# Performance work log

Measured on AMD Instinct MI355X. Metric: run time of the kernel, lower is better.

## Reference

```python
import jax, jax.numpy as jnp
import numpy as np

N_NODES = 16384
N_EDGES = 262144
N_GRAPHS = 64
H = 256          # hidden_dim
DE = 192         # edge feature dim
DG = 64          # g_all dim (DE + DG == H)
NITERS = 3


def _lin(key, fan_in, fan_out):
    kw, kb = jax.random.split(key)
    s = 1.0 / np.sqrt(fan_in)
    return (jax.random.uniform(kw, (fan_in, fan_out), jnp.float32, -s, s),
            jax.random.uniform(kb, (fan_out,), jnp.float32, -s, s))


def setup_inputs() -> dict:
    key = jax.random.key(0)
    ks = jax.random.split(key, 12)
    edge_features = jax.random.normal(ks[0], (N_EDGES, DE), jnp.float32)
    g_all = jax.random.normal(ks[1], (1, DG), jnp.float32)
    edge_index = jax.random.randint(ks[2], (2, N_EDGES), 0, N_NODES, jnp.int32)
    # node_degrees: in-degree per node (what the 1/(1+deg) normalization expects)
    node_degrees = jax.ops.segment_sum(jnp.ones((N_EDGES,), jnp.int32), edge_index[1], num_segments=N_NODES)
    # 64 graphs of 256 nodes each (sorted segment ids, no empty graphs)
    batch = jnp.repeat(jnp.arange(N_GRAPHS, dtype=jnp.int32), N_NODES // N_GRAPHS)
    offs = jnp.arange(N_GRAPHS, dtype=jnp.int32) * (N_NODES // N_GRAPHS)
    heads = offs + jax.random.randint(ks[3], (N_GRAPHS,), 0, N_NODES // N_GRAPHS, jnp.int32)
    tails = offs + jax.random.randint(ks[4], (N_GRAPHS,), 0, N_NODES // N_GRAPHS, jnp.int32)
    ea_w1, ea_b1 = _lin(ks[5], H, H)
    ea_w2, ea_b2 = _lin(ks[6], H, 1)
    eu_w1, eu_b1 = _lin(ks[7], 3 * H + 4, H)
    eu_w2, eu_b2 = _lin(ks[8], H, H)
    gw_w1, gw_b1 = _lin(ks[9], 3 * H, H)
    gw_w2, gw_b2 = _lin(ks[10], H, 1)
    ew_w, ew_b = _lin(ks[11], H, 1)
    return dict(edge_features=edge_features, g_all=g_all,
                ea_w1=ea_w1, ea_b1=ea_b1, ea_w2=ea_w2, ea_b2=ea_b2,
                eu_w1=eu_w1, eu_b1=eu_b1, eu_w2=eu_w2, eu_b2=eu_b2,
                gw_w1=gw_w1, gw_b1=gw_b1, gw_w2=gw_w2, gw_b2=gw_b2,
                ew_w=ew_w, ew_b=ew_b,
                edge_index=edge_index, node_degrees=node_degrees,
                batch=batch, heads=heads, tails=tails)


def reference(edge_features, g_all, ea_w1, ea_b1, ea_w2, ea_b2,
              eu_w1, eu_b1, eu_w2, eu_b2, gw_w1, gw_b1, gw_w2, gw_b2,
              ew_w, ew_b, edge_index, node_degrees, batch, heads, tails):
    src, recv = edge_index[0], edge_index[1]
    E = src.shape[0]
    N = node_degrees.shape[0]
    n_graphs = heads.shape[0]
    dt = edge_features.dtype

    # b_e = cat([edge_features, g_all expanded over edges])
    b_e = jnp.concatenate([edge_features, jnp.broadcast_to(g_all, (E, g_all.shape[1]))], axis=1)

    node_ids = jnp.arange(N)
    is_head = (node_ids == heads[batch]).astype(dt)[:, None]
    is_tail = (node_ids == tails[batch]).astype(dt)[:, None]
    deg = node_degrees.astype(dt)[:, None]

    b_v = jnp.zeros((N, b_e.shape[1]), dt)
    for _ in range(NITERS):
        # per-edge attention score
        score = jax.nn.sigmoid(jax.nn.relu(b_e @ ea_w1 + ea_b1) @ ea_w2 + ea_b2)  # [E,1]
        # scatter_softmax over receiver segments
        m = jax.ops.segment_max(score, recv, num_segments=N)
        ex = jnp.exp(score - m[recv])
        s = jax.ops.segment_sum(ex, recv, num_segments=N)
        alpha = ex / s[recv]
        # scatter_add aggregation + degree normalization
        b_v = jax.ops.segment_sum(alpha * b_e, recv, num_segments=N) / (1.0 + deg)  # [N,H]
        # role-augmented node states, gathered back to edges
        r_v = jnp.concatenate([b_v, is_head, is_tail], axis=1)  # [N,H+2]
        msg = jnp.concatenate([r_v[src], r_v[recv], b_e], axis=1)  # [E,3H+4]
        b_e = jax.nn.relu(msg @ eu_w1 + eu_b1) @ eu_w2 + eu_b2  # [E,H]

    g_max = jax.ops.segment_max(b_v, batch, num_segments=n_graphs)  # [G,H]
    g_G = jnp.concatenate([g_max, b_v[heads], b_v[tails]], axis=1)  # [G,3H]
    w_k = jax.nn.softmax(jax.nn.relu(g_G @ gw_w1 + gw_b1) @ gw_w2 + gw_b2, axis=0)  # [G,1]
    g_all_out = jnp.sum(w_k * g_G, axis=0, keepdims=True)  # [1,3H]
    w_e = jax.nn.sigmoid(b_e @ ew_w + ew_b)  # [E,1]
    return (w_e, g_all_out)
```

## Files before the change

### kernel.cpp

```cpp
#include <hip/hip_runtime.h>
#include <stdint.h>

typedef unsigned short u16;
typedef unsigned int   u32;

#define NN 16384
#define NE 262144
#define NG 64
#define HD 256
#define SHS 264

typedef __attribute__((ext_vector_type(8))) short bfrag;
typedef __attribute__((ext_vector_type(4))) float ffrag;

__device__ __forceinline__ float bf2f(u16 h){
  union { u32 u; float f; } v; v.u = ((u32)h) << 16; return v.f;
}
__device__ __forceinline__ u16 f2bf(float x){
  union { float f; u32 u; } v; v.f = x;
  u32 r = v.u + 0x7fffu + ((v.u >> 16) & 1u);
  return (u16)(r >> 16);
}
__device__ __forceinline__ float sigmoidf(float x){ return 1.f/(1.f+__expf(-x)); }

__device__ __forceinline__ void dma16(const void* g, void* l){
  __builtin_amdgcn_global_load_lds(
      (const __attribute__((address_space(1))) u32*)g,
      (__attribute__((address_space(3))) u32*)l, 16, 0, 0);
}


enum { MODE_SCORE=0, MODE_PQ=4 };

template<int MODE>
__global__ __launch_bounds__(256, 4)
void gemm_k(const u16* __restrict__ A, const u16* __restrict__ Bf0,
            const u16* __restrict__ Bf1,
            float* __restrict__ outF, u16* __restrict__ out0, u16* __restrict__ out1,
            const float* __restrict__ bias, const float* __restrict__ vec,
            const float* __restrict__ scal, const float* __restrict__ flags,
            const float* __restrict__ ht0, const float* __restrict__ ht1)
{
  __shared__ __align__(16) u16 sA[16384];
  __shared__ float sred[4][64];

  const int l  = threadIdx.x & 63;
  const int w  = threadIdx.x >> 6;
  const int q  = l >> 4;
  const int ml = l & 15;
  const long rowBase = (long)blockIdx.x * 64;

  const u16* Bf   = Bf0;
  u16*       outB = out0;
  const float* htp = ht0;
  const float* bp  = bias;
  if (MODE==MODE_PQ && blockIdx.y){ Bf = Bf1; outB = out1; htp = ht1; bp = nullptr; }

  const u16* gA = A + (size_t)(rowBase + w*16 + ml)*HD + q*8;
#pragma unroll
  for (int c=0; c<8; ++c) dma16(gA + c*32, sA + (c*4+w)*512);

  ffrag acc[4][4];
  if constexpr (MODE==MODE_SCORE){
#pragma unroll
    for (int n=0; n<4; ++n){
      const float bb = bias[(w*4+n)*16+ml];
#pragma unroll
      for (int mt=0; mt<4; ++mt) acc[mt][n] = (ffrag){bb,bb,bb,bb};
    }
  } else {
    float h0[4], h1[4], bb[4];
#pragma unroll
    for (int n=0; n<4; ++n){
      const int col = (w*4+n)*16+ml;
      h0[n] = htp[col]; h1[n] = htp[HD+col]; bb[n] = bp ? bp[col] : 0.f;
    }
    float2 fl[16];
#pragma unroll
    for (int i=0; i<16; ++i){
      long row = rowBase + (i>>2)*16 + q*4 + (i&3);
      fl[i] = *(const float2*)(flags + 2*row);
    }
#pragma unroll
    for (int i=0; i<16; ++i){
      const int mt = i>>2, r = i&3;
      const float fh = fl[i].x, ft = fl[i].y;
#pragma unroll
      for (int n=0; n<4; ++n)
        acc[mt][n][r] = bb[n] + fh*h0[n] + ft*h1[n];
    }
  }
  __syncthreads();

  __builtin_amdgcn_s_setprio(1);
#pragma unroll 1
  for (int c=0; c<8; ++c){
    bfrag a[4], b[4];
#pragma unroll
    for (int n=0; n<4; ++n)
      b[n] = *(const bfrag*)(Bf + (((size_t)c*16 + w*4 + n)*64 + l)*8);
#pragma unroll
    for (int mt=0; mt<4; ++mt) a[mt] = *(const bfrag*)(sA + (c*4+mt)*512 + l*8);
#pragma unroll
    for (int mt=0; mt<4; ++mt)
#pragma unroll
      for (int n=0; n<4; ++n)
        acc[mt][n] = __builtin_amdgcn_mfma_f32_16x16x32_bf16(a[mt], b[n], acc[mt][n], 0, 0, 0);
  }
  __builtin_amdgcn_s_setprio(0);

  if constexpr (MODE==MODE_SCORE){
    float part[4][4];
#pragma unroll
    for (int mt=0; mt<4; ++mt)
#pragma unroll
      for (int r=0; r<4; ++r) part[mt][r] = 0.f;
#pragma unroll
    for (int n=0; n<4; ++n){
      const float vvn = vec[(w*4+n)*16+ml];
#pragma unroll
      for (int mt=0; mt<4; ++mt)
#pragma unroll
        for (int r=0; r<4; ++r)
          part[mt][r] += fmaxf(acc[mt][n][r], 0.f) * vvn;
    }
#pragma unroll
    for (int mt=0; mt<4; ++mt)
#pragma unroll
      for (int r=0; r<4; ++r){
        float p = part[mt][r];
        p += __shfl_xor(p, 1, 64); p += __shfl_xor(p, 2, 64);
        p += __shfl_xor(p, 4, 64); p += __shfl_xor(p, 8, 64);
        part[mt][r] = p;
      }
    if (ml == 0)
#pragma unroll
      for (int mt=0; mt<4; ++mt)
#pragma unroll
        for (int r=0; r<4; ++r)
          sred[w][mt*16 + q*4 + r] = part[mt][r];
    __syncthreads();
    if (threadIdx.x < 64){
      const int t = threadIdx.x;
      float v = sred[0][t] + sred[1][t] + sred[2][t] + sred[3][t];
      outF[rowBase + t] = sigmoidf(v + scal[0]);
    }
  } else {
#pragma unroll
    for (int mt=0; mt<4; ++mt)
#pragma unroll
      for (int r=0; r<4; ++r){
        long row = rowBase + mt*16 + q*4 + r;
        u16 o[4];
#pragma unroll
        for (int n=0; n<4; ++n) o[n] = f2bf(acc[mt][n][r]);
        uint2 pk; pk.x = (u32)o[0] | ((u32)o[1]<<16); pk.y = (u32)o[2] | ((u32)o[3]<<16);
        *(uint2*)(outB + (size_t)row*HD + w*64 + ml*4) = pk;
      }
  }
}

template<bool LAST>
__global__ __launch_bounds__(256, 4)
void mega_k(u16* __restrict__ BE, const u16* __restrict__ w1cf,
            const u16* __restrict__ w2f, const u16* __restrict__ eaw1f,
            float* __restrict__ scoreOut, float* __restrict__ weOut,
            const u16* __restrict__ Pg, const u16* __restrict__ Qg,
            const int* __restrict__ srcI, const int* __restrict__ recvI,
            const float* __restrict__ b2,
            const float* __restrict__ sb1, const float* __restrict__ sv,
            const float* __restrict__ ssc,
            const float* __restrict__ wv, const float* __restrict__ wb)
{
  __shared__ __align__(16) u16 sU[64*SHS];
  __shared__ float sred[4][64];
  __shared__ int sIdx[128];

  const int l  = threadIdx.x & 63;
  const int w  = threadIdx.x >> 6;
  const int q  = l >> 4;
  const int ml = l & 15;
  const long rowBase = (long)blockIdx.x * 64;

  const u16* gA = BE + (size_t)(rowBase + w*16 + ml)*HD + q*8;
#pragma unroll
  for (int c=0; c<8; ++c) dma16(gA + c*32, sU + (c*4+w)*512);
  __syncthreads();

  if (threadIdx.x < 128){
    const int t = threadIdx.x;
    sIdx[t] = (t < 64) ? srcI[rowBase + t] : recvI[rowBase + (t - 64)];
  }

  ffrag acc[4][4];
#pragma unroll
  for (int mt=0; mt<4; ++mt)
#pragma unroll
    for (int n=0; n<4; ++n) acc[mt][n] = (ffrag){0.f,0.f,0.f,0.f};

  __builtin_amdgcn_s_setprio(1);
#pragma unroll 1
  for (int c=0; c<8; ++c){
    bfrag a[4], b[4];
#pragma unroll
    for (int n=0; n<4; ++n)
      b[n] = *(const bfrag*)(w1cf + (((size_t)c*16 + w*4 + n)*64 + l)*8);
#pragma unroll
    for (int mt=0; mt<4; ++mt) a[mt] = *(const bfrag*)(sU + (c*4+mt)*512 + l*8);
#pragma unroll
    for (int mt=0; mt<4; ++mt)
#pragma unroll
      for (int n=0; n<4; ++n)
        acc[mt][n] = __builtin_amdgcn_mfma_f32_16x16x32_bf16(a[mt], b[n], acc[mt][n], 0, 0, 0);
  }
  __builtin_amdgcn_s_setprio(0);
  __syncthreads();

#pragma unroll
  for (int mt=0; mt<4; ++mt)
#pragma unroll
    for (int r=0; r<4; ++r){
      const int rl = mt*16 + q*4 + r;
      const int si = sIdx[rl];
      const int ri = sIdx[64 + rl];
      uint2 pu = *(const uint2*)(Pg + (size_t)si*HD + w*64 + ml*4);
      uint2 qu = *(const uint2*)(Qg + (size_t)ri*HD + w*64 + ml*4);
      u16 o[4];
      float pv[4] = { bf2f((u16)(pu.x & 0xffff)), bf2f((u16)(pu.x >> 16)),
                      bf2f((u16)(pu.y & 0xffff)), bf2f((u16)(pu.y >> 16)) };
      float qv[4] = { bf2f((u16)(qu.x & 0xffff)), bf2f((u16)(qu.x >> 16)),
                      bf2f((u16)(qu.y & 0xffff)), bf2f((u16)(qu.y >> 16)) };
#pragma unroll
      for (int n=0; n<4; ++n)
        o[n] = f2bf(fmaxf(acc[mt][n][r] + pv[n] + qv[n], 0.f));
      uint2 pk; pk.x = (u32)o[0] | ((u32)o[1]<<16); pk.y = (u32)o[2] | ((u32)o[3]<<16);
      *(uint2*)(sU + (size_t)rl*SHS + w*64 + ml*4) = pk;
    }
  __syncthreads();

#pragma unroll
  for (int mt=0; mt<4; ++mt)
#pragma unroll
    for (int n=0; n<4; ++n) acc[mt][n] = (ffrag){0.f,0.f,0.f,0.f};
  __builtin_amdgcn_s_setprio(1);
#pragma unroll 1
  for (int c=0; c<8; ++c){
    bfrag a[4], b[4];
#pragma unroll
    for (int n=0; n<4; ++n)
      b[n] = *(const bfrag*)(w2f + (((size_t)c*16 + w*4 + n)*64 + l)*8);
#pragma unroll
    for (int mt=0; mt<4; ++mt)
      a[mt] = *(const bfrag*)(sU + (size_t)(mt*16+ml)*SHS + c*32 + q*8);
#pragma unroll
    for (int mt=0; mt<4; ++mt)
#pragma unroll
      for (int n=0; n<4; ++n)
        acc[mt][n] = __builtin_amdgcn_mfma_f32_16x16x32_bf16(a[mt], b[n], acc[mt][n], 0, 0, 0);
  }
  __builtin_amdgcn_s_setprio(0);

  float bia2[4];
#pragma unroll
  for (int n=0; n<4; ++n) bia2[n] = b2[(w*4+n)*16+ml];

  if constexpr (!LAST){
    __syncthreads();
#pragma unroll
    for (int mt=0; mt<4; ++mt)
#pragma unroll
      for (int r=0; r<4; ++r){
        long row = rowBase + mt*16 + q*4 + r;
        u16 o[4];
#pragma unroll
        for (int n=0; n<4; ++n) o[n] = f2bf(acc[mt][n][r] + bia2[n]);
        uint2 pk; pk.x = (u32)o[0] | ((u32)o[1]<<16); pk.y = (u32)o[2] | ((u32)o[3]<<16);
        *(uint2*)(BE + (size_t)row*HD + w*64 + ml*4) = pk;
        *(uint2*)(sU + (size_t)(mt*16 + q*4 + r)*SHS + w*64 + ml*4) = pk;
      }
    __syncthreads();

#pragma unroll
    for (int mt=0; mt<4; ++mt)
#pragma unroll
      for (int n=0; n<4; ++n) acc[mt][n] = (ffrag){0.f,0.f,0.f,0.f};
    __builtin_amdgcn_s_setprio(1);
#pragma unroll 1
    for (int c=0; c<8; ++c){
      bfrag a[4], b[4];
#pragma unroll
      for (int n=0; n<4; ++n)
        b[n] = *(const bfrag*)(eaw1f + (((size_t)c*16 + w*4 + n)*64 + l)*8);
#pragma unroll
      for (int mt=0; mt<4; ++mt)
        a[mt] = *(const bfrag*)(sU + (size_t)(mt*16+ml)*SHS + c*32 + q*8);
#pragma unroll
      for (int mt=0; mt<4; ++mt)
#pragma unroll
        for (int n=0; n<4; ++n)
          acc[mt][n] = __builtin_amdgcn_mfma_f32_16x16x32_bf16(a[mt], b[n], acc[mt][n], 0, 0, 0);
    }
    __builtin_amdgcn_s_setprio(0);
    float part[4][4];
#pragma unroll
    for (int mt=0; mt<4; ++mt)
#pragma unroll
      for (int r=0; r<4; ++r) part[mt][r] = 0.f;
#pragma unroll
    for (int n=0; n<4; ++n){
      const int col = (w*4+n)*16+ml;
      const float bb = sb1[col], vvn = sv[col];
#pragma unroll
      for (int mt=0; mt<4; ++mt)
#pragma unroll
        for (int r=0; r<4; ++r)
          part[mt][r] += fmaxf(acc[mt][n][r] + bb, 0.f) * vvn;
    }
#pragma unroll
    for (int mt=0; mt<4; ++mt)
#pragma unroll
      for (int r=0; r<4; ++r){
        float p = part[mt][r];
        p += __shfl_xor(p, 1, 64); p += __shfl_xor(p, 2, 64);
        p += __shfl_xor(p, 4, 64); p += __shfl_xor(p, 8, 64);
        part[mt][r] = p;
      }
    if (ml == 0)
#pragma unroll
      for (int mt=0; mt<4; ++mt)
#pragma unroll
        for (int r=0; r<4; ++r)
          sred[w][mt*16 + q*4 + r] = part[mt][r];
    __syncthreads();
    if (threadIdx.x < 64){
      const int t = threadIdx.x;
      float v = sred[0][t] + sred[1][t] + sred[2][t] + sred[3][t];
      scoreOut[rowBase + t] = sigmoidf(v + ssc[0]);
    }
  } else {
    float part[4][4];
#pragma unroll
    for (int mt=0; mt<4; ++mt)
#pragma unroll
      for (int r=0; r<4; ++r) part[mt][r] = 0.f;
#pragma unroll
    for (int n=0; n<4; ++n){
      const float vvn = wv[(w*4+n)*16+ml];
#pragma unroll
      for (int mt=0; mt<4; ++mt)
#pragma unroll
        for (int r=0; r<4; ++r)
          part[mt][r] += (acc[mt][n][r] + bia2[n]) * vvn;
    }
#pragma unroll
    for (int mt=0; mt<4; ++mt)
#pragma unroll
      for (int r=0; r<4; ++r){
        float p = part[mt][r];
        p += __shfl_xor(p, 1, 64); p += __shfl_xor(p, 2, 64);
        p += __shfl_xor(p, 4, 64); p += __shfl_xor(p, 8, 64);
        part[mt][r] = p;
      }
    if (ml == 0)
#pragma unroll
      for (int mt=0; mt<4; ++mt)
#pragma unroll
        for (int r=0; r<4; ++r)
          sred[w][mt*16 + q*4 + r] = part[mt][r];
    __syncthreads();
    if (threadIdx.x < 64){
      const int t = threadIdx.x;
      float v = sred[0][t] + sred[1][t] + sred[2][t] + sred[3][t];
      weOut[rowBase + t] = sigmoidf(v + wb[0]);
    }
  }
}

__global__ void repack_k(const float* __restrict__ B, u16* __restrict__ out){
  int t = blockIdx.x*256 + threadIdx.x;
  int l = t & 63, n = (t>>6)&15, c = t>>10;
  int col = n*16 + (l&15);
  int kbase = c*32 + ((l>>4)<<3);
#pragma unroll
  for (int j=0; j<8; ++j){
    int kp = kbase + j;
    int f = (kp>>6)*64 + (kp&3)*16 + ((kp>>2)&15);
    out[(size_t)t*8 + j] = f2bf(B[(size_t)f*HD + col]);
  }
}

__global__ void initbe_k(const float* __restrict__ ef, const float* __restrict__ gall,
                         u16* __restrict__ BE){
  int t = blockIdx.x*256 + threadIdx.x;
  int e = t >> 6; int p4 = (t & 63) * 4;
  int w64 = p4 >> 6, mlr = (p4 >> 2) & 15;
  u16 o[4];
#pragma unroll
  for (int i=0; i<4; ++i){
    int f = w64*64 + i*16 + mlr;
    float v = (f < 192) ? ef[(size_t)e*192 + f] : gall[f - 192];
    o[i] = f2bf(v);
  }
  uint2 pk; pk.x = (u32)o[0] | ((u32)o[1]<<16); pk.y = (u32)o[2] | ((u32)o[3]<<16);
  *(uint2*)(BE + (size_t)e*HD + p4) = pk;
}

__global__ void flags_k(const int* __restrict__ batch, const int* __restrict__ heads,
                        const int* __restrict__ tails, float* __restrict__ flags){
  int n = blockIdx.x*256 + threadIdx.x;
  int g = batch[n];
  flags[2*n]   = (n == heads[g]) ? 1.f : 0.f;
  flags[2*n+1] = (n == tails[g]) ? 1.f : 0.f;
}

__global__ void scan_k(const int* __restrict__ deg, int* __restrict__ offs,
                       int* __restrict__ cur){
  __shared__ int part[256];
  int tid = threadIdx.x;
  int base = tid * 64;
  int s = 0;
  for (int j=0; j<64; ++j) s += deg[base+j];
  part[tid] = s;
  __syncthreads();
  if (tid == 0){
    int run = 0;
    for (int i=0; i<256; ++i){ int t = part[i]; part[i] = run; run += t; }
  }
  __syncthreads();
  int run = part[tid];
  for (int j=0; j<64; ++j){
    offs[base+j] = run; cur[base+j] = run; run += deg[base+j];
  }
  if (tid == 255) offs[NN] = run;
}

__global__ void fill_k(const int* __restrict__ recv, int* __restrict__ cur,
                       int* __restrict__ eids){
  int e = blockIdx.x*256 + threadIdx.x;
  int r = recv[e];
  int p = atomicAdd(&cur[r], 1);
  eids[p] = e;
}

__global__ __launch_bounds__(256)
void agg_k(const float* __restrict__ score, const u16* __restrict__ BE,
           const int* __restrict__ offs, const int* __restrict__ eids,
           float* __restrict__ bv, u16* __restrict__ bvb){
  int node = blockIdx.x*4 + (threadIdx.x >> 6);
  int l = threadIdx.x & 63;
  int beg = offs[node], end = offs[node+1];

  float m = -1e30f;
  for (int i=beg+l; i<end; i+=64) m = fmaxf(m, score[eids[i]]);
#pragma unroll
  for (int d=1; d<64; d<<=1) m = fmaxf(m, __shfl_xor(m, d, 64));

  float s = 0.f;
  for (int i=beg+l; i<end; i+=64) s += __expf(score[eids[i]] - m);
#pragma unroll
  for (int d=1; d<64; d<<=1) s += __shfl_xor(s, d, 64);

  float deg = (float)(end - beg);
  float scale = (end > beg) ? (1.f/s) * (1.f/(1.f+deg)) : 0.f;

  float a0=0.f, a1=0.f, a2=0.f, a3=0.f;
  for (int i=beg; i<end; ++i){
    int e = eids[i];
    float al = __expf(score[e] - m);
    uint2 uv = *(const uint2*)(BE + (size_t)e*HD + l*4);
    a0 += al * bf2f((u16)(uv.x & 0xffff));
    a1 += al * bf2f((u16)(uv.x >> 16));
    a2 += al * bf2f((u16)(uv.y & 0xffff));
    a3 += al * bf2f((u16)(uv.y >> 16));
  }
  size_t o = (size_t)node*HD + l*4;
  a0 *= scale; a1 *= scale; a2 *= scale; a3 *= scale;
  bv[o+0]=a0; bv[o+1]=a1; bv[o+2]=a2; bv[o+3]=a3;
  uint2 p; p.x = (u32)f2bf(a0) | ((u32)f2bf(a1)<<16);
  p.y = (u32)f2bf(a2) | ((u32)f2bf(a3)<<16);
  *(uint2*)(bvb + o) = p;
}

__global__ void gmax_k(const float* __restrict__ bv, const int* __restrict__ heads,
                       const int* __restrict__ tails, float* __restrict__ gG){
  int g = blockIdx.x, col = threadIdx.x;
  float mx = -1e30f;
  const float* p = bv + (size_t)g*256*HD + col;
  for (int i=0; i<256; ++i) mx = fmaxf(mx, p[(size_t)i*HD]);
  gG[g*768 + col]       = mx;
  gG[g*768 + 256 + col] = bv[(size_t)heads[g]*HD + col];
  gG[g*768 + 512 + col] = bv[(size_t)tails[g]*HD + col];
}

__global__ void glog_k(const float* __restrict__ gG, const float* __restrict__ w1,
                       const float* __restrict__ b1, const float* __restrict__ w2,
                       const float* __restrict__ b2, float* __restrict__ logits){
  int g = blockIdx.x, n = threadIdx.x;
  float a = b1[n];
  const float* gg = gG + g*768;
  for (int k=0; k<768; ++k){
    int b = k >> 8, p = k & 255;
    int f = (p>>6)*64 + (p&3)*16 + ((p>>2)&15);
    a += gg[k] * w1[(size_t)(b*256 + f)*HD + n];
  }
  a = fmaxf(a, 0.f) * w2[n];
#pragma unroll
  for (int d=1; d<64; d<<=1) a += __shfl_xor(a, d, 64);
  __shared__ float red[4];
  if ((threadIdx.x & 63) == 0) red[threadIdx.x >> 6] = a;
  __syncthreads();
  if (threadIdx.x == 0) logits[g] = red[0]+red[1]+red[2]+red[3] + b2[0];
}

__global__ void gfin_k(const float* __restrict__ gG, const float* __restrict__ logits,
                       float* __restrict__ out){
  int tid = threadIdx.x;
  float m = -1e30f;
  for (int g=0; g<NG; ++g) m = fmaxf(m, logits[g]);
  float s = 0.f;
  for (int g=0; g<NG; ++g) s += __expf(logits[g] - m);
  float inv = 1.f/s;
  for (int j=tid; j<768; j+=256){
    int b = j >> 8, f = j & 255;
    int p = (f>>6)*64 + (f&15)*4 + ((f>>4)&3);
    float o = 0.f;
    for (int g=0; g<NG; ++g) o += __expf(logits[g]-m)*inv * gG[g*768 + b*256 + p];
    out[j] = o;
  }
}

extern "C" void kernel_launch(void* const* d_in, const int* in_sizes, int n_in,
                              void* d_out, int out_size, void* d_ws, size_t ws_size,
                              hipStream_t stream)
{
  const float* ef    = (const float*)d_in[0];
  const float* gall  = (const float*)d_in[1];
  const float* ea_w1 = (const float*)d_in[2];
  const float* ea_b1 = (const float*)d_in[3];
  const float* ea_w2 = (const float*)d_in[4];
  const float* ea_b2 = (const float*)d_in[5];
  const float* eu_w1 = (const float*)d_in[6];
  const float* eu_b1 = (const float*)d_in[7];
  const float* eu_w2 = (const float*)d_in[8];
  const float* eu_b2 = (const float*)d_in[9];
  const float* gw_w1 = (const float*)d_in[10];
  const float* gw_b1 = (const float*)d_in[11];
  const float* gw_w2 = (const float*)d_in[12];
  const float* gw_b2 = (const float*)d_in[13];
  const float* ew_w  = (const float*)d_in[14];
  const float* ew_b  = (const float*)d_in[15];
  const int* eidx    = (const int*)d_in[16];
  const int* srcI    = eidx;
  const int* recvI   = eidx + NE;
  const int* ndeg    = (const int*)d_in[17];
  const int* batch   = (const int*)d_in[18];
  const int* heads   = (const int*)d_in[19];
  const int* tails   = (const int*)d_in[20];
  float* out = (float*)d_out;

  char* wsb = (char*)d_ws;
  size_t off = 0;
  auto alloc = [&](size_t sz)->char*{
    char* p = wsb + off; off = (off + sz + 255) & ~(size_t)255; return p;
  };
  u16*   BE    = (u16*)  alloc((size_t)NE*HD*2);
  float* score = (float*)alloc((size_t)NE*4);
  u16*   P     = (u16*)  alloc((size_t)NN*HD*2);
  u16*   Q     = (u16*)  alloc((size_t)NN*HD*2);
  float* bv    = (float*)alloc((size_t)NN*HD*4);
  u16*   bvb   = (u16*)  alloc((size_t)NN*HD*2);
  int*   offs  = (int*)  alloc((size_t)(NN+1)*4);
  int*   cur   = (int*)  alloc((size_t)NN*4);
  int*   eids  = (int*)  alloc((size_t)NE*4);
  float* flags = (float*)alloc((size_t)NN*8);
  u16*   eaw1f = (u16*)  alloc((size_t)65536*2);
  u16*   w1af  = (u16*)  alloc((size_t)65536*2);
  u16*   w1bf  = (u16*)  alloc((size_t)65536*2);
  u16*   w1cf  = (u16*)  alloc((size_t)65536*2);
  u16*   euw2f = (u16*)  alloc((size_t)65536*2);
  float* gG    = (float*)alloc((size_t)NG*768*4);
  float* logits= (float*)alloc((size_t)NG*4);

  repack_k<<<32,256,0,stream>>>(ea_w1, eaw1f);
  repack_k<<<32,256,0,stream>>>(eu_w1, w1af);
  repack_k<<<32,256,0,stream>>>(eu_w1 + 258*HD, w1bf);
  repack_k<<<32,256,0,stream>>>(eu_w1 + 516*HD, w1cf);
  repack_k<<<32,256,0,stream>>>(eu_w2, euw2f);
  initbe_k<<<NE*64/256,256,0,stream>>>(ef, gall, BE);
  flags_k<<<NN/256,256,0,stream>>>(batch, heads, tails, flags);
  scan_k<<<1,256,0,stream>>>(ndeg, offs, cur);
  fill_k<<<NE/256,256,0,stream>>>(recvI, cur, eids);

  gemm_k<MODE_SCORE><<<NE/64,256,0,stream>>>(BE, eaw1f, nullptr, score,
      nullptr, nullptr, ea_b1, ea_w2, ea_b2, nullptr, nullptr, nullptr);

  for (int it=0; it<3; ++it){
    agg_k<<<NN/4,256,0,stream>>>(score, BE, offs, eids, bv, bvb);
    gemm_k<MODE_PQ><<<dim3(NN/64,2),256,0,stream>>>(bvb, w1af, w1bf, nullptr,
        P, Q, eu_b1, nullptr, nullptr, flags, eu_w1 + 256*HD, eu_w1 + 514*HD);
    if (it < 2){
      mega_k<false><<<NE/64,256,0,stream>>>(BE, w1cf, euw2f, eaw1f,
          score, nullptr, P, Q, srcI, recvI, eu_b2,
          ea_b1, ea_w2, ea_b2, nullptr, nullptr);
    } else {
      mega_k<true><<<NE/64,256,0,stream>>>(BE, w1cf, euw2f, eaw1f,
          nullptr, out, P, Q, srcI, recvI, eu_b2,
          nullptr, nullptr, nullptr, ew_w, ew_b);
    }
  }

  gmax_k<<<NG,256,0,stream>>>(bv, heads, tails, gG);
  glog_k<<<NG,256,0,stream>>>(gG, gw_w1, gw_b1, gw_w2, gw_b2, logits);
  gfin_k<<<1,256,0,stream>>>(gG, logits, out + NE);
}
```

Before: 999.1 us.

## Fuse edge-state init with initial score GEMM and use packed bf16 converts

Replaces the separate init kernel and the initial score GEMM with one kernel that reads fp32 edge features, converts them to bf16, writes BE and stages the tile in LDS for the score MFMA. This removes one full write-then-read round trip of the edge state and one launch. Separately, manual bf16 rounding sequences are replaced with the v_cvt_pk_bf16_f32 instruction throughout the epilogues. The fused kernel's feature loads are strided scalar fp32 reads, which may coalesce poorly, and the hardware convert's rounding may differ slightly from the manual routine for special values.

```diff
diff --git a/kernel.cpp b/kernel.cpp
--- a/kernel.cpp
+++ b/kernel.cpp
@@ -20,6 +20,9 @@
   union { float f; u32 u; } v; v.f = x;
   u32 r = v.u + 0x7fffu + ((v.u >> 16) & 1u);
   return (u16)(r >> 16);
+}
+__device__ __forceinline__ u32 cvtpk(float lo, float hi){
+  u32 r; asm("v_cvt_pk_bf16_f32 %0, %1, %2" : "=v"(r) : "v"(lo), "v"(hi)); return r;
 }
 __device__ __forceinline__ float sigmoidf(float x){ return 1.f/(1.f+__expf(-x)); }
 
@@ -151,12 +154,108 @@
 #pragma unroll
       for (int r=0; r<4; ++r){
         long row = rowBase + mt*16 + q*4 + r;
-        u16 o[4];
-#pragma unroll
-        for (int n=0; n<4; ++n) o[n] = f2bf(acc[mt][n][r]);
-        uint2 pk; pk.x = (u32)o[0] | ((u32)o[1]<<16); pk.y = (u32)o[2] | ((u32)o[3]<<16);
+        uint2 pk;
+        pk.x = cvtpk(acc[mt][0][r], acc[mt][1][r]);
+        pk.y = cvtpk(acc[mt][2][r], acc[mt][3][r]);
         *(uint2*)(outB + (size_t)row*HD + w*64 + ml*4) = pk;
       }
+  }
+}
+
+__global__ __launch_bounds__(256, 4)
+void ibs_k(const float* __restrict__ ef, const float* __restrict__ gall,
+           u16* __restrict__ BE, const u16* __restrict__ eaw1f,
+           float* __restrict__ outF,
+           const float* __restrict__ bias, const float* __restrict__ vec,
+           const float* __restrict__ scal)
+{
+  __shared__ __align__(16) u16 sA[16384];
+  __shared__ float sred[4][64];
+
+  const int l  = threadIdx.x & 63;
+  const int w  = threadIdx.x >> 6;
+  const int q  = l >> 4;
+  const int ml = l & 15;
+  const long rowBase = (long)blockIdx.x * 64;
+  const long row = rowBase + w*16 + ml;
+  const float* efr = ef + (size_t)row*192;
+
+  ffrag acc[4][4];
+#pragma unroll
+  for (int n=0; n<4; ++n){
+    const float bb = bias[(w*4+n)*16+ml];
+#pragma unroll
+    for (int mt=0; mt<4; ++mt) acc[mt][n] = (ffrag){bb,bb,bb,bb};
+  }
+
+#pragma unroll
+  for (int c=0; c<8; ++c){
+    float v[8];
+#pragma unroll
+    for (int j=0; j<8; ++j){
+      const int p = c*32 + q*8 + j;
+      const int f = (p>>6)*64 + (p&3)*16 + ((p>>2)&15);
+      v[j] = (c < 6) ? efr[f] : gall[f - 192];
+    }
+    uint4 pk;
+    pk.x = cvtpk(v[0], v[1]); pk.y = cvtpk(v[2], v[3]);
+    pk.z = cvtpk(v[4], v[5]); pk.w = cvtpk(v[6], v[7]);
+    *(uint4*)(sA + (c*4+w)*512 + l*8) = pk;
+    *(uint4*)(BE + (size_t)row*HD + c*32 + q*8) = pk;
+  }
+  __syncthreads();
+
+  __builtin_amdgcn_s_setprio(1);
+#pragma unroll 1
+  for (int c=0; c<8; ++c){
+    bfrag a[4], b[4];
+#pragma unroll
+    for (int n=0; n<4; ++n)
+      b[n] = *(const bfrag*)(eaw1f + (((size_t)c*16 + w*4 + n)*64 + l)*8);
+#pragma unroll
+    for (int mt=0; mt<4; ++mt) a[mt] = *(const bfrag*)(sA + (c*4+mt)*512 + l*8);
+#pragma unroll
+    for (int mt=0; mt<4; ++mt)
+#pragma unroll
+      for (int n=0; n<4; ++n)
+        acc[mt][n] = __builtin_amdgcn_mfma_f32_16x16x32_bf16(a[mt], b[n], acc[mt][n], 0, 0, 0);
+  }
+  __builtin_amdgcn_s_setprio(0);
+
+  float part[4][4];
+#pragma unroll
+  for (int mt=0; mt<4; ++mt)
+#pragma unroll
+    for (int r=0; r<4; ++r) part[mt][r] = 0.f;
+#pragma unroll
+  for (int n=0; n<4; ++n){
+    const float vvn = vec[(w*4+n)*16+ml];
+#pragma unroll
+    for (int mt=0; mt<4; ++mt)
+#pragma unroll
+      for (int r=0; r<4; ++r)
+        part[mt][r] += fmaxf(acc[mt][n][r], 0.f) * vvn;
+  }
+#pragma unroll
+  for (int mt=0; mt<4; ++mt)
+#pragma unroll
+    for (int r=0; r<4; ++r){
+      float p = part[mt][r];
+      p += __shfl_xor(p, 1, 64); p += __shfl_xor(p, 2, 64);
+      p += __shfl_xor(p, 4, 64); p += __shfl_xor(p, 8, 64);
+      part[mt][r] = p;
+    }
+  if (ml == 0)
+#pragma unroll
+    for (int mt=0; mt<4; ++mt)
+#pragma unroll
+      for (int r=0; r<4; ++r)
+        sred[w][mt*16 + q*4 + r] = part[mt][r];
+  __syncthreads();
+  if (threadIdx.x < 64){
+    const int t = threadIdx.x;
+    float v = sred[0][t] + sred[1][t] + sred[2][t] + sred[3][t];
+    outF[rowBase + t] = sigmoidf(v + scal[0]);
   }
 }
 
@@ -225,15 +324,15 @@
       const int ri = sIdx[64 + rl];
       uint2 pu = *(const uint2*)(Pg + (size_t)si*HD + w*64 + ml*4);
       uint2 qu = *(const uint2*)(Qg + (size_t)ri*HD + w*64 + ml*4);
-      u16 o[4];
       float pv[4] = { bf2f((u16)(pu.x & 0xffff)), bf2f((u16)(pu.x >> 16)),
                       bf2f((u16)(pu.y & 0xffff)), bf2f((u16)(pu.y >> 16)) };
       float qv[4] = { bf2f((u16)(qu.x & 0xffff)), bf2f((u16)(qu.x >> 16)),
                       bf2f((u16)(qu.y & 0xffff)), bf2f((u16)(qu.y >> 16)) };
-#pragma unroll
-      for (int n=0; n<4; ++n)
-        o[n] = f2bf(fmaxf(acc[mt][n][r] + pv[n] + qv[n], 0.f));
-      uint2 pk; pk.x = (u32)o[0] | ((u32)o[1]<<16); pk.y = (u32)o[2] | ((u32)o[3]<<16);
+      float v0 = fmaxf(acc[mt][0][r] + pv[0] + qv[0], 0.f);
+      float v1 = fmaxf(acc[mt][1][r] + pv[1] + qv[1], 0.f);
+      float v2 = fmaxf(acc[mt][2][r] + pv[2] + qv[2], 0.f);
+      float v3 = fmaxf(acc[mt][3][r] + pv[3] + qv[3], 0.f);
+      uint2 pk; pk.x = cvtpk(v0, v1); pk.y = cvtpk(v2, v3);
       *(uint2*)(sU + (size_t)rl*SHS + w*64 + ml*4) = pk;
     }
   __syncthreads();
@@ -271,10 +370,9 @@
 #pragma unroll
       for (int r=0; r<4; ++r){
         long row = rowBase + mt*16 + q*4 + r;
-        u16 o[4];
-#pragma unroll
-        for (int n=0; n<4; ++n) o[n] = f2bf(acc[mt][n][r] + bia2[n]);
-        uint2 pk; pk.x = (u32)o[0] | ((u32)o[1]<<16); pk.y = (u32)o[2] | ((u32)o[3]<<16);
+        uint2 pk;
+        pk.x = cvtpk(acc[mt][0][r] + bia2[0], acc[mt][1][r] + bia2[1]);
+        pk.y = cvtpk(acc[mt][2][r] + bia2[2], acc[mt][3][r] + bia2[3]);
         *(uint2*)(BE + (size_t)row*HD + w*64 + ml*4) = pk;
         *(uint2*)(sU + (size_t)(mt*16 + q*4 + r)*SHS + w*64 + ml*4) = pk;
       }
@@ -387,22 +485,6 @@
     int f = (kp>>6)*64 + (kp&3)*16 + ((kp>>2)&15);
     out[(size_t)t*8 + j] = f2bf(B[(size_t)f*HD + col]);
   }
-}
-
-__global__ void initbe_k(const float* __restrict__ ef, const float* __restrict__ gall,
-                         u16* __restrict__ BE){
-  int t = blockIdx.x*256 + threadIdx.x;
-  int e = t >> 6; int p4 = (t & 63) * 4;
-  int w64 = p4 >> 6, mlr = (p4 >> 2) & 15;
-  u16 o[4];
-#pragma unroll
-  for (int i=0; i<4; ++i){
-    int f = w64*64 + i*16 + mlr;
-    float v = (f < 192) ? ef[(size_t)e*192 + f] : gall[f - 192];
-    o[i] = f2bf(v);
-  }
-  uint2 pk; pk.x = (u32)o[0] | ((u32)o[1]<<16); pk.y = (u32)o[2] | ((u32)o[3]<<16);
-  *(uint2*)(BE + (size_t)e*HD + p4) = pk;
 }
 
 __global__ void flags_k(const int* __restrict__ batch, const int* __restrict__ heads,
@@ -476,8 +558,7 @@
   size_t o = (size_t)node*HD + l*4;
   a0 *= scale; a1 *= scale; a2 *= scale; a3 *= scale;
   bv[o+0]=a0; bv[o+1]=a1; bv[o+2]=a2; bv[o+3]=a3;
-  uint2 p; p.x = (u32)f2bf(a0) | ((u32)f2bf(a1)<<16);
-  p.y = (u32)f2bf(a2) | ((u32)f2bf(a3)<<16);
+  uint2 p; p.x = cvtpk(a0, a1); p.y = cvtpk(a2, a3);
   *(uint2*)(bvb + o) = p;
 }
 
@@ -586,13 +667,11 @@
   repack_k<<<32,256,0,stream>>>(eu_w1 + 258*HD, w1bf);
   repack_k<<<32,256,0,stream>>>(eu_w1 + 516*HD, w1cf);
   repack_k<<<32,256,0,stream>>>(eu_w2, euw2f);
-  initbe_k<<<NE*64/256,256,0,stream>>>(ef, gall, BE);
   flags_k<<<NN/256,256,0,stream>>>(batch, heads, tails, flags);
   scan_k<<<1,256,0,stream>>>(ndeg, offs, cur);
   fill_k<<<NE/256,256,0,stream>>>(recvI, cur, eids);
 
-  gemm_k<MODE_SCORE><<<NE/64,256,0,stream>>>(BE, eaw1f, nullptr, score,
-      nullptr, nullptr, ea_b1, ea_w2, ea_b2, nullptr, nullptr, nullptr);
+  ibs_k<<<NE/64,256,0,stream>>>(ef, gall, BE, eaw1f, score, ea_b1, ea_w2, ea_b2);
 
   for (int it=0; it<3; ++it){
     agg_k<<<NN/4,256,0,stream>>>(score, BE, offs, eids, bv, bvb);
```

Measured after the change: 1.016 ms. About the same (+1.7%).
